# Performance work log

Hardware: AMD Instinct MI355X
Metric: run time of the kernel (lower is better)

The kernel has to match this reference:

```python
import jax, jax.numpy as jnp
import numpy as np

OUT, IN, SPEC = 4096, 4096, 512


def _boundprop(last_uA, weight, bias, preact_lb, preact_ub, alpha):
    # simplex_coefficient: relu(W + b[:,None]) - relu(b[:,None]), shape [OUT, IN]
    simplex_coeff = jax.nn.relu(weight + bias[:, None]) - jax.nn.relu(bias[:, None])
    pos_uA = jnp.maximum(last_uA, 0.0)  # [1, SPEC, OUT]
    neg_uA = jnpum if False else jnp.minimum(last_uA, 0.0)

    # ---- simplex branch ----
    lb_u = preact_lb[..., None]  # [1, OUT, 1]
    ub_u = preact_ub[..., None]
    upper_coeff = jnp.where(ub_u <= 0, 0.0, jnp.where(lb_u >= 0, weight, simplex_coeff))  # [1,OUT,IN]
    upper_bias = jnp.where(preact_ub <= 0, 0.0,
                           jnp.where(preact_lb >= 0, bias, jnp.maximum(bias, 0.0)))  # [1,OUT]
    lower_d = (jnp.abs(preact_lb) >= jnp.abs(preact_ub)).astype(last_uA.dtype)  # [1,OUT]
    lower_coeff = jnp.where(ub_u <= 0, 0.0,
                            jnp.where(lb_u >= 0, weight, lower_d[..., None] * weight))  # [1,OUT,IN]
    lower_bias = jnp.where(preact_ub <= 0, 0.0,
                           jnp.where(preact_lb >= 0, bias, lower_d * bias))  # [1,OUT]
    one_minus_a = 1.0 - alpha              # [1,OUT,1]
    one_minus_a_s = 1.0 - alpha[..., 0]    # [1,OUT]
    upper_coeff = one_minus_a * upper_coeff
    lower_coeff = one_minus_a * lower_coeff
    upper_bias = one_minus_a_s * upper_bias
    lower_bias = one_minus_a_s * lower_bias
    simplex_uA = (jnp.einsum('bso,boi->bsi', pos_uA, upper_coeff)
                  + jnp.einsum('bso,boi->bsi', neg_uA, lower_coeff))  # [1,SPEC,IN]
    simplex_ubias = (jnp.einsum('bso,o->bs', pos_uA, upper_bias[0])
                     + jnp.einsum('bso,o->bs', neg_uA, lower_bias[0]))  # [1,SPEC]

    # ---- crown branch ----
    lb_r = jnp.minimum(preact_lb, 0.0)
    ub_r = jnp.maximum(preact_ub, 0.0)
    ub_r = jnp.maximum(ub_r, lb_r + 1e-8)
    upper_d = ub_r / (ub_r - lb_r)  # [1,OUT]
    upper_b = -lb_r * upper_d       # [1,OUT]
    ud = upper_d[:, None, :]        # [1,1,OUT]
    ld = (ud > 0.5).astype(last_uA.dtype)
    crown_uA_pre = ud * pos_uA + ld * neg_uA  # [1,SPEC,OUT]
    crown_ubias = jnp.einsum('bso,bo->bs', pos_uA, upper_b)  # [1,SPEC]
    w = alpha * weight              # [1,OUT,IN]
    b = alpha[..., 0] * bias        # [1,OUT]
    crown_uA = jnp.einsum('bso,boi->bsi', crown_uA_pre, w)   # [1,SPEC,IN]
    crown_ubias = crown_ubias + jnp.einsum('bso,o->bs', crown_uA_pre, b[0])

    return simplex_uA + crown_uA, simplex_ubias + crown_ubias


def setup_inputs() -> dict:
    key = jax.random.key(0)
    k1, k2, k3, k4, k5 = jax.random.split(key, 5)
    weight = jax.random.normal(k1, (OUT, IN), jnp.float32) * 0.02
    bias = jax.random.normal(k2, (OUT,), jnp.float32) * 0.02
    preact_lb = jax.random.normal(k3, (1, OUT), jnp.float32)
    # ensure ub > lb, with mixed-sign ranges so all relaxation branches are hit
    preact_ub = preact_lb + jnp.abs(jax.random.normal(k4, (1, OUT), jnp.float32)) + 1e-2
    last_uA = jax.random.normal(k5, (1, SPEC, OUT), jnp.float32)
    alpha = jnp.ones((1, OUT, 1), jnp.float32)
    return {'last_uA': last_uA, 'weight': weight, 'bias': bias,
            'preact_lb': preact_lb, 'preact_ub': preact_ub, 'alpha': alpha}


def reference(last_uA, weight, bias, preact_lb, preact_ub, alpha):
    uA, ubias = _boundprop(last_uA, weight, bias, preact_lb, preact_ub, alpha)
    return uA, ubias
```

## Files before the change

### kernel.cpp

```cpp
#include <hip/hip_runtime.h>
#include <hip/hip_bf16.h>
#include <stdint.h>

#define OUTN 4096
#define INN  4096
#define SPECN 512

typedef __attribute__((ext_vector_type(8))) short short8;
typedef __attribute__((ext_vector_type(4))) float f32x4;

__device__ __forceinline__ ushort f2bf(float f) {
    uint32_t u = __float_as_uint(f);
    uint32_t r = (u + 0x7FFFu + ((u >> 16) & 1u)) >> 16;
    return (ushort)r;
}

__global__ __launch_bounds__(256) void build_A(
    const float* __restrict__ uA, const float* __restrict__ Lb,
    const float* __restrict__ Ub, const float* __restrict__ Bias,
    const float* __restrict__ Alpha, ushort* __restrict__ A1,
    ushort* __restrict__ A2, float* __restrict__ ubias_out)
{
    const int s = blockIdx.x;
    const int tid = threadIdx.x;
    float acc = 0.f;

    for (int p = 0; p < 4; ++p) {
        const int o = p * 1024 + tid * 4;
        const float4 u4 = *(const float4*)&uA[(size_t)s * OUTN + o];
        const float4 lb4 = *(const float4*)&Lb[o];
        const float4 ub4 = *(const float4*)&Ub[o];
        const float4 b4 = *(const float4*)&Bias[o];
        const float4 a4 = *(const float4*)&Alpha[o];
        const float uu[4] = {u4.x, u4.y, u4.z, u4.w};
        const float lbv[4] = {lb4.x, lb4.y, lb4.z, lb4.w};
        const float ubv[4] = {ub4.x, ub4.y, ub4.z, ub4.w};
        const float bv[4] = {b4.x, b4.y, b4.z, b4.w};
        const float av[4] = {a4.x, a4.y, a4.z, a4.w};
        ushort r1[4], r2[4];
#pragma unroll
        for (int j = 0; j < 4; ++j) {
            const float u = uu[j], lb = lbv[j], ub = ubv[j], b = bv[j], a = av[j];
            const float pp = fmaxf(u, 0.f), nn = fminf(u, 0.f);
            const bool stneg = (ub <= 0.f);
            const bool stpos = (lb >= 0.f);
            const float lower_d = (fabsf(lb) >= fabsf(ub)) ? 1.f : 0.f;
            float lbr = fminf(lb, 0.f);
            float ubr = fmaxf(ub, 0.f);
            ubr = fmaxf(ubr, lbr + 1e-8f);
            const float ud = ubr / (ubr - lbr);
            const float upb = -lbr * ud;
            const float ldc = (ud > 0.5f) ? 1.f : 0.f;
            const float oma = 1.f - a;
            const float crown = ud * pp + ldc * nn;
            const float wcoef = a * crown +
                oma * (stneg ? 0.f : (stpos ? (pp + nn) : lower_d * nn));
            const float scoef = (stneg || stpos) ? 0.f : oma * pp;
            const float ub_t = stneg ? 0.f : (stpos ? b : fmaxf(b, 0.f));
            const float lb_t = stneg ? 0.f : (stpos ? b : lower_d * b);
            acc += pp * (oma * ub_t + upb) + nn * (oma * lb_t) + crown * (a * b);
            r1[j] = f2bf(wcoef);
            r2[j] = f2bf(scoef);
        }
        *(ushort4*)&A1[(size_t)s * OUTN + o] = make_ushort4(r1[0], r1[1], r1[2], r1[3]);
        *(ushort4*)&A2[(size_t)s * OUTN + o] = make_ushort4(r2[0], r2[1], r2[2], r2[3]);
    }

#pragma unroll
    for (int off = 32; off > 0; off >>= 1) acc += __shfl_down(acc, off);
    __shared__ float red[4];
    if ((tid & 63) == 0) red[tid >> 6] = acc;
    __syncthreads();
    if (tid == 0) ubias_out[s] = red[0] + red[1] + red[2] + red[3];
}

__global__ __launch_bounds__(256) void make_flags(
    const ushort* __restrict__ A2, int* __restrict__ flags)
{
    const int b = blockIdx.x;
    const int tid = threadIdx.x;
    const int c0 = b * 64 + (tid & 15) * 4;
    const int rbase = tid >> 4;
    int any = 0;
    for (int k = 0; k < 32; ++k) {
        const int r = rbase + k * 16;
        const ushort4 v = *(const ushort4*)&A2[(size_t)r * OUTN + c0];
        any |= (v.x & 0x7FFF) | (v.y & 0x7FFF) | (v.z & 0x7FFF) | (v.w & 0x7FFF);
    }
    __shared__ int f;
    if (tid == 0) f = 0;
    __syncthreads();
    if (__any(any != 0) && (tid & 63) == 0) atomicOr(&f, 1);
    __syncthreads();
    if (tid == 0) flags[b] = f;
}

__global__ __launch_bounds__(256) void transpose_w(
    const float* __restrict__ W, const float* __restrict__ Bias,
    const int* __restrict__ flags, ushort* __restrict__ WT,
    ushort* __restrict__ ST)
{
    __shared__ float t[64][65];
    const int bi = blockIdx.x & 63;
    const int bo = blockIdx.x >> 6;
    const int i0 = bi * 64, o0 = bo * 64;
    const int tid = threadIdx.x;
    const bool needS = (flags[bo] != 0);
    const int sub = tid >> 4;
    const int q4 = (tid & 15) * 4;

#pragma unroll
    for (int p = 0; p < 4; ++p) {
        const int ol = p * 16 + sub;
        const float4 w = *(const float4*)&W[(size_t)(o0 + ol) * INN + i0 + q4];
        t[q4 + 0][ol] = w.x;
        t[q4 + 1][ol] = w.y;
        t[q4 + 2][ol] = w.z;
        t[q4 + 3][ol] = w.w;
    }
    __syncthreads();
#pragma unroll
    for (int p = 0; p < 4; ++p) {
        const int il = p * 16 + sub;
        const float w0 = t[il][q4], w1 = t[il][q4 + 1];
        const float w2 = t[il][q4 + 2], w3 = t[il][q4 + 3];
        *(ushort4*)&WT[(size_t)(i0 + il) * OUTN + o0 + q4] =
            make_ushort4(f2bf(w0), f2bf(w1), f2bf(w2), f2bf(w3));
        if (needS) {
            const float4 b4 = *(const float4*)&Bias[o0 + q4];
            const float s0 = fmaxf(w0 + b4.x, 0.f) - fmaxf(b4.x, 0.f);
            const float s1 = fmaxf(w1 + b4.y, 0.f) - fmaxf(b4.y, 0.f);
            const float s2 = fmaxf(w2 + b4.z, 0.f) - fmaxf(b4.z, 0.f);
            const float s3 = fmaxf(w3 + b4.w, 0.f) - fmaxf(b4.w, 0.f);
            *(ushort4*)&ST[(size_t)(i0 + il) * OUTN + o0 + q4] =
                make_ushort4(f2bf(s0), f2bf(s1), f2bf(s2), f2bf(s3));
        }
    }
}

__global__ __launch_bounds__(256) void gemm(
    const ushort* __restrict__ A1, const ushort* __restrict__ A2,
    const ushort* __restrict__ WT, const ushort* __restrict__ ST,
    const int* __restrict__ flags, float* __restrict__ outp)
{
    __shared__ ushort sA1[64 * 64];
    __shared__ ushort sB[64 * 64];
    __shared__ ushort sA2[64 * 64];
    __shared__ ushort sS[64 * 64];

    const int bx = blockIdx.x & 63;
    const int by = blockIdx.x >> 6;
    const int i0 = bx * 64, s0 = by * 64;
    const int tid = threadIdx.x;
    const int lane = tid & 63;
    const int w = tid >> 6;
    const int wr = w >> 1, wc = w & 1;

    f32x4 acc[2][2] = {};

    const int rA[2] = { (w * 2 + 0) * 8 + (lane >> 3), (w * 2 + 1) * 8 + (lane >> 3) };
    const int gcol[2] = { (lane & 7) ^ (rA[0] & 7), (lane & 7) ^ (rA[1] & 7) };

    for (int ko = 0; ko < OUTN; ko += 64) {
        const bool useS = (flags[ko >> 6] != 0);
#pragma unroll
        for (int h = 0; h < 2; ++h) {
            const int c = w * 2 + h;
            const int r = rA[h];
            const size_t goff = (size_t)ko + gcol[h] * 8;
            __builtin_amdgcn_global_load_lds(
                (const __attribute__((address_space(1))) void*)(A1 + (size_t)(s0 + r) * OUTN + goff),
                (__attribute__((address_space(3))) void*)&sA1[c * 512], 16, 0, 0);
            __builtin_amdgcn_global_load_lds(
                (const __attribute__((address_space(1))) void*)(WT + (size_t)(i0 + r) * OUTN + goff),
                (__attribute__((address_space(3))) void*)&sB[c * 512], 16, 0, 0);
            if (useS) {
                __builtin_amdgcn_global_load_lds(
                    (const __attribute__((address_space(1))) void*)(A2 + (size_t)(s0 + r) * OUTN + goff),
                    (__attribute__((address_space(3))) void*)&sA2[c * 512], 16, 0, 0);
                __builtin_amdgcn_global_load_lds(
                    (const __attribute__((address_space(1))) void*)(ST + (size_t)(i0 + r) * OUTN + goff),
                    (__attribute__((address_space(3))) void*)&sS[c * 512], 16, 0, 0);
            }
        }
        __syncthreads();

#pragma unroll
        for (int kk = 0; kk < 64; kk += 32) {
            short8 av[2], bv[2];
#pragma unroll
            for (int m = 0; m < 2; ++m) {
                const int r = wr * 32 + m * 16 + (lane & 15);
                const int g = ((kk >> 3) + (lane >> 4)) ^ (r & 7);
                av[m] = *(const short8*)&sA1[r * 64 + g * 8];
            }
#pragma unroll
            for (int n = 0; n < 2; ++n) {
                const int r = wc * 32 + n * 16 + (lane & 15);
                const int g = ((kk >> 3) + (lane >> 4)) ^ (r & 7);
                bv[n] = *(const short8*)&sB[r * 64 + g * 8];
            }
#pragma unroll
            for (int m = 0; m < 2; ++m)
#pragma unroll
                for (int n = 0; n < 2; ++n)
                    acc[m][n] = __builtin_amdgcn_mfma_f32_16x16x32_bf16(
                        av[m], bv[n], acc[m][n], 0, 0, 0);
            if (useS) {
                short8 av2[2], bv2[2];
#pragma unroll
                for (int m = 0; m < 2; ++m) {
                    const int r = wr * 32 + m * 16 + (lane & 15);
                    const int g = ((kk >> 3) + (lane >> 4)) ^ (r & 7);
                    av2[m] = *(const short8*)&sA2[r * 64 + g * 8];
                }
#pragma unroll
                for (int n = 0; n < 2; ++n) {
                    const int r = wc * 32 + n * 16 + (lane & 15);
                    const int g = ((kk >> 3) + (lane >> 4)) ^ (r & 7);
                    bv2[n] = *(const short8*)&sS[r * 64 + g * 8];
                }
#pragma unroll
                for (int m = 0; m < 2; ++m)
#pragma unroll
                    for (int n = 0; n < 2; ++n)
                        acc[m][n] = __builtin_amdgcn_mfma_f32_16x16x32_bf16(
                            av2[m], bv2[n], acc[m][n], 0, 0, 0);
            }
        }
        __syncthreads();
    }

#pragma unroll
    for (int m = 0; m < 2; ++m)
#pragma unroll
        for (int n = 0; n < 2; ++n) {
            const int srow = s0 + wr * 32 + m * 16 + (lane >> 4) * 4;
            const int icol = i0 + wc * 32 + n * 16 + (lane & 15);
#pragma unroll
            for (int r = 0; r < 4; ++r)
                outp[(size_t)(srow + r) * INN + icol] = acc[m][n][r];
        }
}

extern "C" void kernel_launch(void* const* d_in, const int* in_sizes, int n_in,
                              void* d_out, int out_size, void* d_ws, size_t ws_size,
                              hipStream_t stream) {
    const float* uA    = (const float*)d_in[0];
    const float* W     = (const float*)d_in[1];
    const float* Bias  = (const float*)d_in[2];
    const float* Lb    = (const float*)d_in[3];
    const float* Ub    = (const float*)d_in[4];
    const float* Alpha = (const float*)d_in[5];
    float* outp = (float*)d_out;

    char* ws = (char*)d_ws;
    int*    flags = (int*)ws;
    ushort* A1 = (ushort*)(ws + 4096);
    ushort* A2 = (ushort*)(ws + 4096 + (1u << 22));
    ushort* WT = (ushort*)(ws + 4096 + (2u << 22));
    ushort* ST = (ushort*)(ws + 4096 + (2u << 22) + (1u << 25));

    build_A<<<512, 256, 0, stream>>>(uA, Lb, Ub, Bias, Alpha, A1, A2,
                                     outp + (size_t)SPECN * INN);
    make_flags<<<64, 256, 0, stream>>>(A2, flags);
    transpose_w<<<4096, 256, 0, stream>>>(W, Bias, flags, WT, ST);
    gemm<<<512, 256, 0, stream>>>(A1, A2, WT, ST, flags, outp);
}
```

Baseline: 164.2 us.

## Fuse prep kernels, compute simplex coeffs on the fly, double-buffer GEMM

Folds build_A, flag generation and the weight transpose into a single prep launch, with per-row masks of active simplex K-blocks replacing the separate make_flags pass. The materialized simplex-coefficient matrix ST is dropped; the GEMM recomputes relu(W+b)-relu(b) from bf16 W in registers, and only for K-blocks the mask marks active. The main GEMM loop now uses BK=128 with double-buffered LDS staging and swizzled block ordering for L2 reuse. This removes two launches and the ST write and read, at the cost of extra ALU work and an extra bf16 rounding of W before the simplex transform, which can change numerics slightly.

```diff
diff --git a/kernel.cpp b/kernel.cpp
--- a/kernel.cpp
+++ b/kernel.cpp
@@ -5,6 +5,8 @@
 #define OUTN 4096
 #define INN  4096
 #define SPECN 512
+#define BK 128
+#define KT (OUTN / BK)
 
 typedef __attribute__((ext_vector_type(8))) short short8;
 typedef __attribute__((ext_vector_type(4))) float f32x4;
@@ -14,191 +16,164 @@
     uint32_t r = (u + 0x7FFFu + ((u >> 16) & 1u)) >> 16;
     return (ushort)r;
 }
-
-__global__ __launch_bounds__(256) void build_A(
-    const float* __restrict__ uA, const float* __restrict__ Lb,
-    const float* __restrict__ Ub, const float* __restrict__ Bias,
-    const float* __restrict__ Alpha, ushort* __restrict__ A1,
-    ushort* __restrict__ A2, float* __restrict__ ubias_out)
+__device__ __forceinline__ float bf2f(ushort u) {
+    return __uint_as_float((uint32_t)u << 16);
+}
+
+__global__ __launch_bounds__(256) void prep(
+    const float* __restrict__ uA, const float* __restrict__ W,
+    const float* __restrict__ Bias, const float* __restrict__ Lb,
+    const float* __restrict__ Ub, const float* __restrict__ Alpha,
+    ushort* __restrict__ A1, ushort* __restrict__ A2, ushort* __restrict__ WT,
+    unsigned long long* __restrict__ rowmask, float* __restrict__ ubias_out)
 {
-    const int s = blockIdx.x;
     const int tid = threadIdx.x;
-    float acc = 0.f;
-
-    for (int p = 0; p < 4; ++p) {
-        const int o = p * 1024 + tid * 4;
-        const float4 u4 = *(const float4*)&uA[(size_t)s * OUTN + o];
-        const float4 lb4 = *(const float4*)&Lb[o];
-        const float4 ub4 = *(const float4*)&Ub[o];
-        const float4 b4 = *(const float4*)&Bias[o];
-        const float4 a4 = *(const float4*)&Alpha[o];
-        const float uu[4] = {u4.x, u4.y, u4.z, u4.w};
-        const float lbv[4] = {lb4.x, lb4.y, lb4.z, lb4.w};
-        const float ubv[4] = {ub4.x, ub4.y, ub4.z, ub4.w};
-        const float bv[4] = {b4.x, b4.y, b4.z, b4.w};
-        const float av[4] = {a4.x, a4.y, a4.z, a4.w};
-        ushort r1[4], r2[4];
-#pragma unroll
-        for (int j = 0; j < 4; ++j) {
-            const float u = uu[j], lb = lbv[j], ub = ubv[j], b = bv[j], a = av[j];
-            const float pp = fmaxf(u, 0.f), nn = fminf(u, 0.f);
-            const bool stneg = (ub <= 0.f);
-            const bool stpos = (lb >= 0.f);
-            const float lower_d = (fabsf(lb) >= fabsf(ub)) ? 1.f : 0.f;
-            float lbr = fminf(lb, 0.f);
-            float ubr = fmaxf(ub, 0.f);
-            ubr = fmaxf(ubr, lbr + 1e-8f);
-            const float ud = ubr / (ubr - lbr);
-            const float upb = -lbr * ud;
-            const float ldc = (ud > 0.5f) ? 1.f : 0.f;
-            const float oma = 1.f - a;
-            const float crown = ud * pp + ldc * nn;
-            const float wcoef = a * crown +
-                oma * (stneg ? 0.f : (stpos ? (pp + nn) : lower_d * nn));
-            const float scoef = (stneg || stpos) ? 0.f : oma * pp;
-            const float ub_t = stneg ? 0.f : (stpos ? b : fmaxf(b, 0.f));
-            const float lb_t = stneg ? 0.f : (stpos ? b : lower_d * b);
-            acc += pp * (oma * ub_t + upb) + nn * (oma * lb_t) + crown * (a * b);
-            r1[j] = f2bf(wcoef);
-            r2[j] = f2bf(scoef);
-        }
-        *(ushort4*)&A1[(size_t)s * OUTN + o] = make_ushort4(r1[0], r1[1], r1[2], r1[3]);
-        *(ushort4*)&A2[(size_t)s * OUTN + o] = make_ushort4(r2[0], r2[1], r2[2], r2[3]);
-    }
-
-#pragma unroll
-    for (int off = 32; off > 0; off >>= 1) acc += __shfl_down(acc, off);
-    __shared__ float red[4];
-    if ((tid & 63) == 0) red[tid >> 6] = acc;
-    __syncthreads();
-    if (tid == 0) ubias_out[s] = red[0] + red[1] + red[2] + red[3];
-}
-
-__global__ __launch_bounds__(256) void make_flags(
-    const ushort* __restrict__ A2, int* __restrict__ flags)
-{
-    const int b = blockIdx.x;
-    const int tid = threadIdx.x;
-    const int c0 = b * 64 + (tid & 15) * 4;
-    const int rbase = tid >> 4;
-    int any = 0;
-    for (int k = 0; k < 32; ++k) {
-        const int r = rbase + k * 16;
-        const ushort4 v = *(const ushort4*)&A2[(size_t)r * OUTN + c0];
-        any |= (v.x & 0x7FFF) | (v.y & 0x7FFF) | (v.z & 0x7FFF) | (v.w & 0x7FFF);
-    }
-    __shared__ int f;
-    if (tid == 0) f = 0;
-    __syncthreads();
-    if (__any(any != 0) && (tid & 63) == 0) atomicOr(&f, 1);
-    __syncthreads();
-    if (tid == 0) flags[b] = f;
-}
-
-__global__ __launch_bounds__(256) void transpose_w(
-    const float* __restrict__ W, const float* __restrict__ Bias,
-    const int* __restrict__ flags, ushort* __restrict__ WT,
-    ushort* __restrict__ ST)
-{
-    __shared__ float t[64][65];
-    const int bi = blockIdx.x & 63;
-    const int bo = blockIdx.x >> 6;
-    const int i0 = bi * 64, o0 = bo * 64;
-    const int tid = threadIdx.x;
-    const bool needS = (flags[bo] != 0);
-    const int sub = tid >> 4;
-    const int q4 = (tid & 15) * 4;
-
-#pragma unroll
-    for (int p = 0; p < 4; ++p) {
-        const int ol = p * 16 + sub;
-        const float4 w = *(const float4*)&W[(size_t)(o0 + ol) * INN + i0 + q4];
-        t[q4 + 0][ol] = w.x;
-        t[q4 + 1][ol] = w.y;
-        t[q4 + 2][ol] = w.z;
-        t[q4 + 3][ol] = w.w;
-    }
-    __syncthreads();
-#pragma unroll
-    for (int p = 0; p < 4; ++p) {
-        const int il = p * 16 + sub;
-        const float w0 = t[il][q4], w1 = t[il][q4 + 1];
-        const float w2 = t[il][q4 + 2], w3 = t[il][q4 + 3];
-        *(ushort4*)&WT[(size_t)(i0 + il) * OUTN + o0 + q4] =
-            make_ushort4(f2bf(w0), f2bf(w1), f2bf(w2), f2bf(w3));
-        if (needS) {
-            const float4 b4 = *(const float4*)&Bias[o0 + q4];
-            const float s0 = fmaxf(w0 + b4.x, 0.f) - fmaxf(b4.x, 0.f);
-            const float s1 = fmaxf(w1 + b4.y, 0.f) - fmaxf(b4.y, 0.f);
-            const float s2 = fmaxf(w2 + b4.z, 0.f) - fmaxf(b4.z, 0.f);
-            const float s3 = fmaxf(w3 + b4.w, 0.f) - fmaxf(b4.w, 0.f);
-            *(ushort4*)&ST[(size_t)(i0 + il) * OUTN + o0 + q4] =
-                make_ushort4(f2bf(s0), f2bf(s1), f2bf(s2), f2bf(s3));
+    if (blockIdx.x < 512) {
+        const int s = blockIdx.x;
+        float acc = 0.f;
+        unsigned long long msk = 0;
+        for (int p = 0; p < 4; ++p) {
+            const int o = p * 1024 + tid * 4;
+            const float4 u4 = *(const float4*)&uA[(size_t)s * OUTN + o];
+            const float4 lb4 = *(const float4*)&Lb[o];
+            const float4 ub4 = *(const float4*)&Ub[o];
+            const float4 b4 = *(const float4*)&Bias[o];
+            const float4 a4 = *(const float4*)&Alpha[o];
+            const float uu[4] = {u4.x, u4.y, u4.z, u4.w};
+            const float lbv[4] = {lb4.x, lb4.y, lb4.z, lb4.w};
+            const float ubv[4] = {ub4.x, ub4.y, ub4.z, ub4.w};
+            const float bv[4] = {b4.x, b4.y, b4.z, b4.w};
+            const float av[4] = {a4.x, a4.y, a4.z, a4.w};
+            ushort r1[4], r2[4];
+#pragma unroll
+            for (int j = 0; j < 4; ++j) {
+                const float u = uu[j], lb = lbv[j], ub = ubv[j], b = bv[j], a = av[j];
+                const float pp = fmaxf(u, 0.f), nn = fminf(u, 0.f);
+                const bool stneg = (ub <= 0.f);
+                const bool stpos = (lb >= 0.f);
+                const float lower_d = (fabsf(lb) >= fabsf(ub)) ? 1.f : 0.f;
+                float lbr = fminf(lb, 0.f);
+                float ubr = fmaxf(ub, 0.f);
+                ubr = fmaxf(ubr, lbr + 1e-8f);
+                const float ud = ubr / (ubr - lbr);
+                const float upb = -lbr * ud;
+                const float ldc = (ud > 0.5f) ? 1.f : 0.f;
+                const float oma = 1.f - a;
+                const float crown = ud * pp + ldc * nn;
+                const float wcoef = a * crown +
+                    oma * (stneg ? 0.f : (stpos ? (pp + nn) : lower_d * nn));
+                const float scoef = (stneg || stpos) ? 0.f : oma * pp;
+                const float ub_t = stneg ? 0.f : (stpos ? b : fmaxf(b, 0.f));
+                const float lb_t = stneg ? 0.f : (stpos ? b : lower_d * b);
+                acc += pp * (oma * ub_t + upb) + nn * (oma * lb_t) + crown * (a * b);
+                r1[j] = f2bf(wcoef);
+                r2[j] = f2bf(scoef);
+            }
+            *(ushort4*)&A1[(size_t)s * OUTN + o] = make_ushort4(r1[0], r1[1], r1[2], r1[3]);
+            *(ushort4*)&A2[(size_t)s * OUTN + o] = make_ushort4(r2[0], r2[1], r2[2], r2[3]);
+            if (((r2[0] | r2[1] | r2[2] | r2[3]) & 0x7FFF) != 0)
+                msk |= 1ull << (p * 16 + (tid >> 4));
+        }
+#pragma unroll
+        for (int off = 32; off; off >>= 1) {
+            acc += __shfl_down(acc, off);
+            msk |= __shfl_down(msk, off);
+        }
+        __shared__ float redf[4];
+        __shared__ unsigned long long redm[4];
+        if ((tid & 63) == 0) { redf[tid >> 6] = acc; redm[tid >> 6] = msk; }
+        __syncthreads();
+        if (tid == 0) {
+            ubias_out[s] = redf[0] + redf[1] + redf[2] + redf[3];
+            rowmask[s] = redm[0] | redm[1] | redm[2] | redm[3];
+        }
+    } else {
+        __shared__ float t[64][65];
+        const int tb = blockIdx.x - 512;
+        const int bi = tb & 63, bo = tb >> 6;
+        const int i0 = bi * 64, o0 = bo * 64;
+        const int sub = tid >> 4;
+        const int q4 = (tid & 15) * 4;
+#pragma unroll
+        for (int p = 0; p < 4; ++p) {
+            const int ol = p * 16 + sub;
+            const float4 w = *(const float4*)&W[(size_t)(o0 + ol) * INN + i0 + q4];
+            t[q4 + 0][ol] = w.x;
+            t[q4 + 1][ol] = w.y;
+            t[q4 + 2][ol] = w.z;
+            t[q4 + 3][ol] = w.w;
+        }
+        __syncthreads();
+#pragma unroll
+        for (int p = 0; p < 4; ++p) {
+            const int il = p * 16 + sub;
+            *(ushort4*)&WT[(size_t)(i0 + il) * OUTN + o0 + q4] =
+                make_ushort4(f2bf(t[il][q4]), f2bf(t[il][q4 + 1]),
+                             f2bf(t[il][q4 + 2]), f2bf(t[il][q4 + 3]));
         }
     }
 }
 
 __global__ __launch_bounds__(256) void gemm(
     const ushort* __restrict__ A1, const ushort* __restrict__ A2,
-    const ushort* __restrict__ WT, const ushort* __restrict__ ST,
-    const int* __restrict__ flags, float* __restrict__ outp)
+    const ushort* __restrict__ WT, const float* __restrict__ Bias,
+    const unsigned long long* __restrict__ rowmask, float* __restrict__ outp)
 {
-    __shared__ ushort sA1[64 * 64];
-    __shared__ ushort sB[64 * 64];
-    __shared__ ushort sA2[64 * 64];
-    __shared__ ushort sS[64 * 64];
-
-    const int bx = blockIdx.x & 63;
-    const int by = blockIdx.x >> 6;
+    __shared__ ushort sA[2][64 * BK];
+    __shared__ ushort sB[2][64 * BK];
+    __shared__ unsigned long long smaskLds;
+
+    const int bid = blockIdx.x;
+    const int swz = (bid & 7) * 64 + (bid >> 3);
+    const int bx = swz >> 3;
+    const int by = swz & 7;
     const int i0 = bx * 64, s0 = by * 64;
     const int tid = threadIdx.x;
     const int lane = tid & 63;
     const int w = tid >> 6;
     const int wr = w >> 1, wc = w & 1;
 
+    if (tid < 64) {
+        unsigned long long v = rowmask[s0 + tid];
+#pragma unroll
+        for (int off = 32; off; off >>= 1) v |= __shfl_down(v, off);
+        if (tid == 0) smaskLds = v;
+    }
+
     f32x4 acc[2][2] = {};
 
-    const int rA[2] = { (w * 2 + 0) * 8 + (lane >> 3), (w * 2 + 1) * 8 + (lane >> 3) };
-    const int gcol[2] = { (lane & 7) ^ (rA[0] & 7), (lane & 7) ^ (rA[1] & 7) };
-
-    for (int ko = 0; ko < OUTN; ko += 64) {
-        const bool useS = (flags[ko >> 6] != 0);
-#pragma unroll
-        for (int h = 0; h < 2; ++h) {
-            const int c = w * 2 + h;
-            const int r = rA[h];
-            const size_t goff = (size_t)ko + gcol[h] * 8;
+    auto stage = [&](int buf, int t) {
+        const int ko = t * BK;
+#pragma unroll
+        for (int h = 0; h < 4; ++h) {
+            const int c = w * 4 + h;
+            const int r = c * 4 + (lane >> 4);
+            const int g = (lane & 15) ^ (r & 15);
+            const size_t off = (size_t)ko + g * 8;
             __builtin_amdgcn_global_load_lds(
-                (const __attribute__((address_space(1))) void*)(A1 + (size_t)(s0 + r) * OUTN + goff),
-                (__attribute__((address_space(3))) void*)&sA1[c * 512], 16, 0, 0);
+                (const __attribute__((address_space(1))) void*)(A1 + (size_t)(s0 + r) * OUTN + off),
+                (__attribute__((address_space(3))) void*)&sA[buf][c * 512], 16, 0, 0);
             __builtin_amdgcn_global_load_lds(
-                (const __attribute__((address_space(1))) void*)(WT + (size_t)(i0 + r) * OUTN + goff),
-                (__attribute__((address_space(3))) void*)&sB[c * 512], 16, 0, 0);
-            if (useS) {
-                __builtin_amdgcn_global_load_lds(
-                    (const __attribute__((address_space(1))) void*)(A2 + (size_t)(s0 + r) * OUTN + goff),
-                    (__attribute__((address_space(3))) void*)&sA2[c * 512], 16, 0, 0);
-                __builtin_amdgcn_global_load_lds(
-                    (const __attribute__((address_space(1))) void*)(ST + (size_t)(i0 + r) * OUTN + goff),
-                    (__attribute__((address_space(3))) void*)&sS[c * 512], 16, 0, 0);
-            }
-        }
-        __syncthreads();
-
-#pragma unroll
-        for (int kk = 0; kk < 64; kk += 32) {
+                (const __attribute__((address_space(1))) void*)(WT + (size_t)(i0 + r) * OUTN + off),
+                (__attribute__((address_space(3))) void*)&sB[buf][c * 512], 16, 0, 0);
+        }
+    };
+
+    auto compute = [&](int buf) {
+#pragma unroll
+        for (int kk = 0; kk < BK; kk += 32) {
             short8 av[2], bv[2];
 #pragma unroll
             for (int m = 0; m < 2; ++m) {
                 const int r = wr * 32 + m * 16 + (lane & 15);
-                const int g = ((kk >> 3) + (lane >> 4)) ^ (r & 7);
-                av[m] = *(const short8*)&sA1[r * 64 + g * 8];
+                const int g = ((kk >> 3) + (lane >> 4)) ^ (r & 15);
+                av[m] = *(const short8*)&sA[buf][r * BK + g * 8];
             }
 #pragma unroll
             for (int n = 0; n < 2; ++n) {
                 const int r = wc * 32 + n * 16 + (lane & 15);
-                const int g = ((kk >> 3) + (lane >> 4)) ^ (r & 7);
-                bv[n] = *(const short8*)&sB[r * 64 + g * 8];
+                const int g = ((kk >> 3) + (lane >> 4)) ^ (r & 15);
+                bv[n] = *(const short8*)&sB[buf][r * BK + g * 8];
             }
 #pragma unroll
             for (int m = 0; m < 2; ++m)
@@ -206,29 +181,71 @@
                 for (int n = 0; n < 2; ++n)
                     acc[m][n] = __builtin_amdgcn_mfma_f32_16x16x32_bf16(
                         av[m], bv[n], acc[m][n], 0, 0, 0);
-            if (useS) {
-                short8 av2[2], bv2[2];
+        }
+    };
+
+    stage(0, 0);
+    __syncthreads();
+    const unsigned long long smask = smaskLds;
+    for (int t = 0; t < KT - 1; ++t) {
+        stage((t + 1) & 1, t + 1);
+        compute(t & 1);
+        __syncthreads();
+    }
+    compute((KT - 1) & 1);
+
+    if (smask) {
+        for (int b = 0; b < 64; ++b) {
+            if (!((smask >> b) & 1)) continue;
+            __syncthreads();
+#pragma unroll
+            for (int h = 0; h < 2; ++h) {
+                const int c = w * 2 + h;
+                const int r = c * 8 + (lane >> 3);
+                const int g = (lane & 7) ^ (r & 7);
+                const size_t off = (size_t)b * 64 + g * 8;
+                __builtin_amdgcn_global_load_lds(
+                    (const __attribute__((address_space(1))) void*)(A2 + (size_t)(s0 + r) * OUTN + off),
+                    (__attribute__((address_space(3))) void*)&sA[0][c * 512], 16, 0, 0);
+                __builtin_amdgcn_global_load_lds(
+                    (const __attribute__((address_space(1))) void*)(WT + (size_t)(i0 + r) * OUTN + off),
+                    (__attribute__((address_space(3))) void*)&sB[0][c * 512], 16, 0, 0);
+            }
+            __syncthreads();
+#pragma unroll
+            for (int kk = 0; kk < 64; kk += 32) {
+                short8 av2[2], bw[2];
 #pragma unroll
                 for (int m = 0; m < 2; ++m) {
                     const int r = wr * 32 + m * 16 + (lane & 15);
                     const int g = ((kk >> 3) + (lane >> 4)) ^ (r & 7);
-                    av2[m] = *(const short8*)&sA2[r * 64 + g * 8];
+                    av2[m] = *(const short8*)&sA[0][r * 64 + g * 8];
                 }
+                const int kb = kk + (lane >> 4) * 8;
+                const float4 b0 = *(const float4*)&Bias[b * 64 + kb];
+                const float4 b1 = *(const float4*)&Bias[b * 64 + kb + 4];
+                const float bb[8] = {b0.x, b0.y, b0.z, b0.w, b1.x, b1.y, b1.z, b1.w};
 #pragma unroll
                 for (int n = 0; n < 2; ++n) {
                     const int r = wc * 32 + n * 16 + (lane & 15);
                     const int g = ((kk >> 3) + (lane >> 4)) ^ (r & 7);
-                    bv2[n] = *(const short8*)&sS[r * 64 + g * 8];
+                    const short8 wv = *(const short8*)&sB[0][r * 64 + g * 8];
+                    short8 sv;
+#pragma unroll
+                    for (int j = 0; j < 8; ++j) {
+                        const float wf = bf2f((ushort)wv[j]);
+                        sv[j] = (short)f2bf(fmaxf(wf + bb[j], 0.f) - fmaxf(bb[j], 0.f));
+                    }
+                    bw[n] = sv;
                 }
 #pragma unroll
                 for (int m = 0; m < 2; ++m)
 #pragma unroll
                     for (int n = 0; n < 2; ++n)
                         acc[m][n] = __builtin_amdgcn_mfma_f32_16x16x32_bf16(
-                            av2[m], bv2[n], acc[m][n], 0, 0, 0);
-            }
-        }
-        __syncthreads();
+                            av2[m], bw[n], acc[m][n], 0, 0, 0);
+            }
+        }
     }
 
 #pragma unroll
@@ -255,15 +272,12 @@
     float* outp = (float*)d_out;
 
     char* ws = (char*)d_ws;
-    int*    flags = (int*)ws;
+    unsigned long long* rowmask = (unsigned long long*)ws;
     ushort* A1 = (ushort*)(ws + 4096);
     ushort* A2 = (ushort*)(ws + 4096 + (1u << 22));
     ushort* WT = (ushort*)(ws + 4096 + (2u << 22));
-    ushort* ST = (ushort*)(ws + 4096 + (2u << 22) + (1u << 25));
-
-    build_A<<<512, 256, 0, stream>>>(uA, Lb, Ub, Bias, Alpha, A1, A2,
-                                     outp + (size_t)SPECN * INN);
-    make_flags<<<64, 256, 0, stream>>>(A2, flags);
-    transpose_w<<<4096, 256, 0, stream>>>(W, Bias, flags, WT, ST);
-    gemm<<<512, 256, 0, stream>>>(A1, A2, WT, ST, flags, outp);
-}
+
+    prep<<<4608, 256, 0, stream>>>(uA, W, Bias, Lb, Ub, Alpha, A1, A2, WT,
+                                   rowmask, outp + (size_t)SPECN * INN);
+    gemm<<<512, 256, 0, stream>>>(A1, A2, WT, Bias, rowmask, outp);
+}
```

Result: faster. 146.6 us (-10.7%).
